# Kernel tuning notes

Hardware: AMD Instinct MI355X
Metric: run time of the kernel (lower is better)

The kernel has to match this reference:

```python
import jax, jax.numpy as jnp
import numpy as np

WS = 8          # window_size
POOL = 7        # int(sqrt(agent_num=49)) -> AdaptiveAvgPool1d output size


def _pool_matrix(L, p):
    """Averaging matrix [L, p] replicating torch AdaptiveAvgPool1d(L -> p)."""
    starts = np.floor(np.arange(p) * L / p).astype(int)
    ends = np.ceil((np.arange(p) + 1) * L / p).astype(int)
    P = np.zeros((L, p), dtype=np.float32)
    for i in range(p):
        P[starts[i]:ends[i], i] = 1.0 / (ends[i] - starts[i])
    return jnp.asarray(P)


def setup_inputs() -> dict:
    key = jax.random.key(0)
    ks = jax.random.split(key, 4)
    B, C, H, W = 8, 96, 192, 192
    s = 1.0 / np.sqrt(C)
    return {
        "x": jax.random.normal(ks[0], (B, C, H, W), jnp.float32),
        "Wv": jax.random.normal(ks[1], (C, C), jnp.float32) * s,
        "bv": jnp.zeros((C,), jnp.float32),
        "Wq": jax.random.normal(ks[2], (C, C), jnp.float32) * s,
        "bq": jnp.zeros((C,), jnp.float32),
        "Wk": jax.random.normal(ks[3], (C, C), jnp.float32) * s,
        "bk": jnp.zeros((C,), jnp.float32),
    }


def _conv1x1(x, Wt, b):
    # Conv2d(dim, dim, 1): weight [out, in]
    return jnp.einsum('bchw,oc->bohw', x, Wt) + b[None, :, None, None]


def reference(x, Wv, bv, Wq, bq, Wk, bk):
    B, C, H, W = x.shape
    ws = WS
    nh, nw = H // ws, W // ws
    L = ws * ws  # tokens per window (64)

    v = _conv1x1(x, Wv, bv)
    q = _conv1x1(x, Wq, bq)
    k = _conv1x1(x, Wk, bk)

    def win(t):  # b c (h dh) (w dw) -> (b h w) (dh dw) c
        t = t.reshape(B, C, nh, ws, nw, ws)
        return t.transpose(0, 2, 4, 3, 5, 1).reshape(B * nh * nw, L, C)

    vw, qw, kw = win(v), win(q), win(k)  # (N, 64, C) each

    # agent tokens: adaptive avg pool over the 64 in-window positions -> 7
    P = _pool_matrix(L, POOL)
    agent = jnp.einsum('nlc,lp->npc', qw, P)  # (N, 7, C)

    # agent attention (attn_drop = 0 -> identity)
    a_attn = jax.nn.softmax(jnp.einsum('npc,nlc->npl', agent, kw), axis=-1)
    agent_v = jnp.einsum('npl,nlc->npc', a_attn, vw)            # (N, 7, C)
    q_attn = jax.nn.softmax(jnp.einsum('nlc,npc->nlp', qw, agent), axis=-1)
    f = jnp.einsum('nlp,npc->nlc', q_attn, agent_v)             # (N, 64, C)

    # (b h w) (dh dw) c -> b c (h dh) (w dw)
    out = f.reshape(B, nh, nw, ws, ws, C).transpose(0, 5, 1, 3, 2, 4)
    return out.reshape(B, C, H, W)
```

## Files before the change

### kernel.cpp

```cpp
#include <hip/hip_runtime.h>


constexpr int C_   = 96;
constexpr int Wimg = 192;
constexpr int HWp  = 192 * 192;
constexpr int NWIN = 24;
constexpr int Pp   = 7;

typedef __attribute__((ext_vector_type(8))) __bf16 bf16x8;
typedef __attribute__((ext_vector_type(4))) __bf16 bf16x4;
typedef __attribute__((ext_vector_type(8))) short  short8;
typedef __attribute__((ext_vector_type(4))) float  f32x4;
union frag_u { short8 s; bf16x8 b; };

constexpr int XWS   = 0;
constexpr int RA    = 12288;
constexpr int XPH   = RA;
constexpr int XPL   = RA + 1600;
constexpr int LRAW  = RA;
constexpr int RB    = 16512;
constexpr int GKQH  = RB;
constexpr int GKQL  = RB + 3200;
constexpr int AVH   = RB;
constexpr int AVL   = RB + 1536;
constexpr int QATH  = 22912;
constexpr int QATL  = 23936;
constexpr int BIAS  = 24960;
constexpr int SMEMB = 25024;

constexpr int WS_FRAG_BYTE = 18944 * 4;
constexpr int WS_WV_BYTE   = WS_FRAG_BYTE + 84 * 1024;


__device__ __forceinline__ void bar() {
    asm volatile("s_waitcnt lgkmcnt(0)" ::: "memory");
    __builtin_amdgcn_s_barrier();
}

__device__ __forceinline__ short8 xws_fragA(const unsigned char* S, int mt, int ks, int lane) {
    const int c  = mt * 16 + (lane & 15);
    const int l2 = ks * 64 + ((lane >> 4) << 4);
    return *reinterpret_cast<const short8*>(S + XWS + c * 128 + (l2 ^ ((c & 7) << 4)));
}

__device__ __forceinline__ void pack_hilo4(unsigned char* S, int hi_off, int lo_off,
                                           const f32x4 acc) {
    bf16x4 h, l;
    #pragma unroll
    for (int i = 0; i < 4; ++i) {
        h[i] = (__bf16)acc[i];
        l[i] = (__bf16)(acc[i] - (float)h[i]);
    }
    *reinterpret_cast<bf16x4*>(S + hi_off) = h;
    *reinterpret_cast<bf16x4*>(S + lo_off) = l;
}


__global__ void precompute_mv(const float* __restrict__ Wq,
                              const float* __restrict__ Wk,
                              const float* __restrict__ bq,
                              const float* __restrict__ bk,
                              float* __restrict__ Mk,  float* __restrict__ Mq,
                              float* __restrict__ uk,  float* __restrict__ uq,
                              float* __restrict__ bk2, float* __restrict__ bq2,
                              float* __restrict__ scal)
{
    const int bid = blockIdx.x;
    if (bid < 96) {
        const int c  = bid;
        const int cp = threadIdx.x;
        float ak = 0.f, aq = 0.f;
        for (int a = 0; a < C_; ++a) {
            const float wq = Wq[a * C_ + c];
            ak = fmaf(wq, Wk[a * C_ + cp], ak);
            aq = fmaf(wq, Wq[a * C_ + cp], aq);
        }
        Mk[c * C_ + cp] = ak;
        Mq[c * C_ + cp] = aq;
    } else {
        const int c = threadIdx.x;
        float a_uk = 0.f, a_uq = 0.f, a_bk2 = 0.f, a_bq2 = 0.f;
        for (int a = 0; a < C_; ++a) {
            const float wqc = Wq[a * C_ + c];
            a_uk  = fmaf(wqc, bk[a], a_uk);
            a_uq  = fmaf(wqc, bq[a], a_uq);
            a_bk2 = fmaf(bq[a], Wk[a * C_ + c], a_bk2);
            a_bq2 = fmaf(bq[a], Wq[a * C_ + c], a_bq2);
        }
        uk[c] = a_uk; uq[c] = a_uq; bk2[c] = a_bk2; bq2[c] = a_bq2;
        if (c == 0) {
            float sk = 0.f, sq = 0.f;
            for (int a = 0; a < C_; ++a) { sk += bq[a] * bk[a]; sq += bq[a] * bq[a]; }
            scal[0] = sk; scal[1] = sq;
        }
    }
}

__global__ void precompute_frags(const float* __restrict__ ws,
                                 const float* __restrict__ Wv,
                                 unsigned char* __restrict__ wsb)
{
    const int bid = blockIdx.x, lane = threadIdx.x;
    short8 o;
    if (bid < 84) {
        const int hl = bid & 1, ks = (bid >> 1) % 3, nt = (bid / 6) % 7, mat = bid / 42;
        const float* M = ws + (mat ? 9216 : 0);
        const float* u = ws + (mat ? 18528 : 18432);
        const int col = nt * 16 + (lane & 15);
        #pragma unroll
        for (int j = 0; j < 8; ++j) {
            const int k = ks * 32 + (lane >> 4) * 8 + j;
            const float raw = (col < 96) ? M[k * 96 + col] : ((col == 96) ? u[k] : 0.f);
            const __bf16 hi = (__bf16)raw;
            union { __bf16 h; short s; } cv;
            cv.h = hl ? (__bf16)(raw - (float)hi) : hi;
            o[j] = cv.s;
        }
        *reinterpret_cast<short8*>(wsb + WS_FRAG_BYTE + bid * 1024 + lane * 16) = o;
    } else {
        const int wb = bid - 84;
        const int hl = wb & 1, ks = (wb >> 1) % 3, mt = wb / 6;
        const int row = mt * 16 + (lane & 15);
        #pragma unroll
        for (int j = 0; j < 8; ++j) {
            const int c = ks * 32 + (lane >> 4) * 8 + j;
            const float raw = Wv[row * 96 + c];
            const __bf16 hi = (__bf16)raw;
            union { __bf16 h; short s; } cv;
            cv.h = hl ? (__bf16)(raw - (float)hi) : hi;
            o[j] = cv.s;
        }
        *reinterpret_cast<short8*>(wsb + WS_WV_BYTE + wb * 1024 + lane * 16) = o;
    }
}

#define LOADPAIR(dstH, dstL, tab, slot_h) do {                                               \
    (dstH).s = *reinterpret_cast<const short8*>((tab) + (slot_h) * 1024 + (lane << 4));      \
    (dstL).s = *reinterpret_cast<const short8*>((tab) + ((slot_h) + 1) * 1024 + (lane << 4));\
} while (0)


__global__ __launch_bounds__(256, 5) void camixer_main(
    const float* __restrict__ x,
    const float* __restrict__ bv,
    const float* __restrict__ bk2,
    const float* __restrict__ bq2,
    const float* __restrict__ scal,
    const unsigned char* __restrict__ mfrag,
    const unsigned char* __restrict__ wvfrag,
    float* __restrict__ out)
{
    __shared__ __align__(16) unsigned char S[SMEMB];
    float* Lraw   = (float*)(S + LRAW);
    float* bias16 = (float*)(S + BIAS);

    const int t = threadIdx.x;
    const int lane = t & 63, w = t >> 6;
    const int wid = ((blockIdx.x & 7) * 576) + (blockIdx.x >> 3);
    const int b  = wid / (NWIN * NWIN);
    const int r  = wid % (NWIN * NWIN);
    const int h0 = (r / NWIN) * 8;
    const int w0 = (r % NWIN) * 8;
    const int base = b * C_ * HWp + h0 * Wimg + w0;
    const float scal0 = scal[0], scal1 = scal[1];
    const short8 zero8 = {0, 0, 0, 0, 0, 0, 0, 0};

    frag_u B0h[3], B0l[3];
    LOADPAIR(B0h[0], B0l[0], mfrag, (w * 3 + 0) * 2);
    LOADPAIR(B0h[1], B0l[1], mfrag, (w * 3 + 1) * 2);
    LOADPAIR(B0h[2], B0l[2], mfrag, (w * 3 + 2) * 2);

    {
        const float4* x4 = reinterpret_cast<const float4*>(x);
        #pragma unroll
        for (int rr = 0; rr < 2; ++rr) {
            const int idx = t + (rr << 8);
            if (idx < 384) {
                const int dw4 = idx & 1;
                const int dh  = (idx >> 1) & 7;
                const int c4  = idx >> 4;
                const int c0 = c4 * 4, l0 = dh * 8 + dw4 * 4;
                #pragma unroll
                for (int j = 0; j < 4; ++j) {
                    const int c = c0 + j;
                    const float4 v = x4[(base + c * HWp + dh * Wimg + dw4 * 4) >> 2];
                    bf16x4 d = {(__bf16)v.x, (__bf16)v.y, (__bf16)v.z, (__bf16)v.w};
                    *reinterpret_cast<bf16x4*>(S + XWS + c * 128 + ((l0 * 2) ^ ((c & 7) << 4))) = d;
                }
            }
        }
    }
    bar();

    {
        frag_u PBh[2], PBl[2];
        {
            const int p = lane & 15;
            const __bf16 PH = (__bf16)0.1f;
            const __bf16 PL = (__bf16)(0.1f - (float)PH);
            const int sp = (p < 7) ? ((p << 6) / 7) : 1000;
            #pragma unroll
            for (int ks = 0; ks < 2; ++ks)
                #pragma unroll
                for (int j = 0; j < 8; ++j) {
                    const int l = ks * 32 + (lane >> 4) * 8 + j;
                    const bool in = (l >= sp) && (l < sp + 10);
                    PBh[ks].b[j] = in ? PH : (__bf16)0.f;
                    PBl[ks].b[j] = in ? PL : (__bf16)0.f;
                }
        }
        #pragma unroll
        for (int rnd = 0; rnd < 2; ++rnd) {
            const int mt = rnd ? (4 + w) : w;
            if (rnd == 0 || w < 2) {
                f32x4 acc = {0.f, 0.f, 0.f, 0.f};
                #pragma unroll
                for (int ks = 0; ks < 2; ++ks) {
                    frag_u A;
                    A.s = xws_fragA(S, mt, ks, lane);
                    acc = __builtin_amdgcn_mfma_f32_16x16x32_bf16(A.b, PBh[ks].b, acc, 0, 0, 0);
                    acc = __builtin_amdgcn_mfma_f32_16x16x32_bf16(A.b, PBl[ks].b, acc, 0, 0, 0);
                }
                const int p = lane & 15;
                if (p < 8) {
                    const int c0 = mt * 16 + (lane >> 4) * 4;
                    pack_hilo4(S, XPH + p * 200 + c0 * 2, XPL + p * 200 + c0 * 2, acc);
                }
            }
        }
    }
    bar();

    {
        frag_u Bh[3], Bl[3];
        #pragma unroll
        for (int ks = 0; ks < 3; ++ks) {
            const int off = ((lane & 15) & 7) * 200 + (ks * 32 + (lane >> 4) * 8) * 2;
            Bh[ks].s = *reinterpret_cast<const short8*>(S + XPH + off);
            Bl[ks].s = *reinterpret_cast<const short8*>(S + XPL + off);
        }

        #define G0TILE(TT, AH, AL) do {                                               \
            const int tt_ = (TT);                                                     \
            const int mat_ = (tt_ >= 7) ? 1 : 0;                                      \
            const int nt_  = tt_ - 7 * mat_;                             \
            f32x4 acc = {0.f, 0.f, 0.f, 0.f};                                         \
            acc = __builtin_amdgcn_mfma_f32_16x16x32_bf16(AH[0].b, Bh[0].b, acc, 0,0,0); \
            acc = __builtin_amdgcn_mfma_f32_16x16x32_bf16(AL[0].b, Bh[0].b, acc, 0,0,0); \
            acc = __builtin_amdgcn_mfma_f32_16x16x32_bf16(AH[0].b, Bl[0].b, acc, 0,0,0); \
            acc = __builtin_amdgcn_mfma_f32_16x16x32_bf16(AH[1].b, Bh[1].b, acc, 0,0,0); \
            acc = __builtin_amdgcn_mfma_f32_16x16x32_bf16(AL[1].b, Bh[1].b, acc, 0,0,0); \
            acc = __builtin_amdgcn_mfma_f32_16x16x32_bf16(AH[1].b, Bl[1].b, acc, 0,0,0); \
            acc = __builtin_amdgcn_mfma_f32_16x16x32_bf16(AH[2].b, Bh[2].b, acc, 0,0,0); \
            acc = __builtin_amdgcn_mfma_f32_16x16x32_bf16(AL[2].b, Bh[2].b, acc, 0,0,0); \
            acc = __builtin_amdgcn_mfma_f32_16x16x32_bf16(AH[2].b, Bl[2].b, acc, 0,0,0); \
            const int p_ = lane & 15;                                    \
            if (nt_ < 6) {                                                            \
                if (p_ < 8) {                                                         \
                    const int cp0_ = nt_ * 16 + (lane >> 4) * 4;                      \
                    const float4 b4_ = *reinterpret_cast<const float4*>(              \
                        (mat_ ? bq2 : bk2) + cp0_);                                   \
                    f32x4 av_;                                                        \
                    av_[0] = acc[0] + b4_.x; av_[1] = acc[1] + b4_.y;                 \
                    av_[2] = acc[2] + b4_.z; av_[3] = acc[3] + b4_.w;                 \
                    const int pr_ = p_ + 8 * mat_;                                    \
                    pack_hilo4(S, GKQH + pr_ * 200 + cp0_ * 2,                        \
                               GKQL + pr_ * 200 + cp0_ * 2, av_);                     \
                }                                                                     \
            } else if ((lane >> 4) == 0 && p_ < 8) {                                  \
                bias16[p_ + 8 * mat_] = acc[0];             \
            }                                                                         \
        } while (0)

        frag_u B1h[3], B1l[3], B2h[3], B2l[3], B3h[3], B3l[3];
        LOADPAIR(B1h[0], B1l[0], mfrag, ((w + 4) * 3 + 0) * 2);
        LOADPAIR(B1h[1], B1l[1], mfrag, ((w + 4) * 3 + 1) * 2);
        LOADPAIR(B1h[2], B1l[2], mfrag, ((w + 4) * 3 + 2) * 2);
        G0TILE(w, B0h, B0l);
        LOADPAIR(B2h[0], B2l[0], mfrag, ((w + 8) * 3 + 0) * 2);
        LOADPAIR(B2h[1], B2l[1], mfrag, ((w + 8) * 3 + 1) * 2);
        LOADPAIR(B2h[2], B2l[2], mfrag, ((w + 8) * 3 + 2) * 2);
        G0TILE(w + 4, B1h, B1l);
        if (w < 2) {
            LOADPAIR(B3h[0], B3l[0], mfrag, ((w + 12) * 3 + 0) * 2);
            LOADPAIR(B3h[1], B3l[1], mfrag, ((w + 12) * 3 + 1) * 2);
            LOADPAIR(B3h[2], B3l[2], mfrag, ((w + 12) * 3 + 2) * 2);
        }
        G0TILE(w + 8, B2h, B2l);
        if (w < 2) G0TILE(w + 12, B3h, B3l);
        #undef G0TILE
    }
    bar();

    {
        frag_u B[3];
        {
            const int l2 = (w * 16 + (lane & 15)) * 2;
            const int kb = (lane >> 4) << 10;
            #pragma unroll
            for (int j = 0; j < 8; ++j) {
                const int aj = kb + j * 128 + (l2 ^ (j << 4));
                B[0].b[j] = *reinterpret_cast<const __bf16*>(S + XWS + aj);
                B[1].b[j] = *reinterpret_cast<const __bf16*>(S + XWS + 4096 + aj);
                B[2].b[j] = *reinterpret_cast<const __bf16*>(S + XWS + 8192 + aj);
            }
        }
        frag_u Ah[3], Al[3];
        #pragma unroll
        for (int ks = 0; ks < 3; ++ks) {
            const int off = (lane & 15) * 200 + (ks * 32 + (lane >> 4) * 8) * 2;
            Ah[ks].s = *reinterpret_cast<const short8*>(S + GKQH + off);
            Al[ks].s = *reinterpret_cast<const short8*>(S + GKQL + off);
        }
        f32x4 acc = {0.f, 0.f, 0.f, 0.f};
        #pragma unroll
        for (int ks = 0; ks < 3; ++ks) {
            acc = __builtin_amdgcn_mfma_f32_16x16x32_bf16(Ah[ks].b, B[ks].b, acc, 0, 0, 0);
            acc = __builtin_amdgcn_mfma_f32_16x16x32_bf16(Al[ks].b, B[ks].b, acc, 0, 0, 0);
        }
        const int colL = w * 16 + (lane & 15);
        const int g = lane >> 4;
        if (g < 2) {
            #pragma unroll
            for (int rr = 0; rr < 4; ++rr) {
                const int pr = g * 4 + rr;
                Lraw[pr * 66 + colL] = acc[rr] + bias16[pr] + scal0;
            }
        } else {
            const bool isg3 = (g == 3);
            float v[4];
            #pragma unroll
            for (int rr = 0; rr < 4; ++rr)
                v[rr] = acc[rr] + bias16[8 + (g - 2) * 4 + rr] + scal1;
            float mymax = fmaxf(fmaxf(v[0], v[1]), isg3 ? v[2] : fmaxf(v[2], v[3]));
            const float omax = __shfl_xor(mymax, 16);
            const float mx = fmaxf(mymax, omax);
            float e[4];
            e[0] = __expf(v[0] - mx); e[1] = __expf(v[1] - mx); e[2] = __expf(v[2] - mx);
            e[3] = isg3 ? 0.f : __expf(v[3] - mx);
            float mysum = (e[0] + e[1]) + (e[2] + e[3]);
            const float osum = __shfl_xor(mysum, 16);
            const float inv = 1.f / (mysum + osum);
            float a[4], pa[4];
            #pragma unroll
            for (int rr = 0; rr < 4; ++rr) a[rr] = e[rr] * inv;
            #pragma unroll
            for (int rr = 0; rr < 4; ++rr) pa[rr] = __shfl_xor(a[rr], 16);
            if (!isg3) {
                frag_u qh, ql;
                #pragma unroll
                for (int p = 0; p < 4; ++p) {
                    const __bf16 hb = (__bf16)a[p];
                    qh.b[p] = hb; ql.b[p] = (__bf16)(a[p] - (float)hb);
                }
                #pragma unroll
                for (int p = 0; p < 4; ++p) {
                    const __bf16 hb = (__bf16)pa[p];
                    qh.b[4 + p] = hb; ql.b[4 + p] = (__bf16)(pa[p] - (float)hb);
                }
                *reinterpret_cast<short8*>(S + QATH + colL * 16) = qh.s;
                *reinterpret_cast<short8*>(S + QATL + colL * 16) = ql.s;
            }
        }
    }
    bar();

    {
        const int nrows = (w < 3) ? 2 : 1;
        #pragma unroll
        for (int rr = 0; rr < 2; ++rr) {
            if (rr < nrows) {
                const int pp = (w < 3) ? (w + 3 * rr) : 6;
                const float v = Lraw[pp * 66 + lane];
                float mx = v;
                #pragma unroll
                for (int off = 32; off; off >>= 1) mx = fmaxf(mx, __shfl_xor(mx, off));
                const float e = __expf(v - mx);
                float s = e;
                #pragma unroll
                for (int off = 32; off; off >>= 1) s += __shfl_xor(s, off);
                const float a = e / s;
                const __bf16 hb = (__bf16)a;
                const __bf16 lb = (__bf16)(a - (float)hb);
                const int ks = lane >> 5;
                const int off_b = ((pp + 16 * ((lane >> 3) & 3)) << 4) + ((lane & 7) << 1);
                *reinterpret_cast<__bf16*>(S + RB + (ks << 10) + off_b) = hb;
                *reinterpret_cast<__bf16*>(S + RB + ((2 + ks) << 10) + off_b) = lb;
            }
        }
    }
    bar();

    frag_u V0h[3], V0l[3], V1h[3], V1l[3];
    {
        LOADPAIR(V0h[0], V0l[0], wvfrag, (w * 3 + 0) * 2);
        LOADPAIR(V0h[1], V0l[1], wvfrag, (w * 3 + 1) * 2);
        LOADPAIR(V0h[2], V0l[2], wvfrag, (w * 3 + 2) * 2);
        if (w < 2) {
            LOADPAIR(V1h[0], V1l[0], wvfrag, ((4 + w) * 3 + 0) * 2);
            LOADPAIR(V1h[1], V1l[1], wvfrag, ((4 + w) * 3 + 1) * 2);
            LOADPAIR(V1h[2], V1l[2], wvfrag, ((4 + w) * 3 + 2) * 2);
        }

        frag_u Bh[2], Bl[2];
        #pragma unroll
        for (int ks = 0; ks < 2; ++ks) {
            Bh[ks].s = *reinterpret_cast<const short8*>(S + RB + (ks << 10) + (lane << 4));
            Bl[ks].s = *reinterpret_cast<const short8*>(S + RB + ((2 + ks) << 10) + (lane << 4));
        }
        const int mt0 = (w < 2) ? w * 2 : (w + 2);
        const int nmt = (w < 2) ? 2 : 1;
        for (int m = 0; m < nmt; ++m) {
            const int mt = mt0 + m;
            f32x4 acc = {0.f, 0.f, 0.f, 0.f};
            #pragma unroll
            for (int ks = 0; ks < 2; ++ks) {
                frag_u A;
                A.s = xws_fragA(S, mt, ks, lane);
                acc = __builtin_amdgcn_mfma_f32_16x16x32_bf16(A.b, Bh[ks].b, acc, 0, 0, 0);
                acc = __builtin_amdgcn_mfma_f32_16x16x32_bf16(A.b, Bl[ks].b, acc, 0, 0, 0);
            }
            const int p = lane & 15;
            if (p < 8) {
                const int c0 = mt * 16 + (lane >> 4) * 4;
                pack_hilo4(S, XPH + p * 200 + c0 * 2, XPL + p * 200 + c0 * 2, acc);
            }
        }
    }
    bar();

    {
        const bool row7 = ((lane & 15) & 7) == 7;
        frag_u Ah[3], Al[3];
        #pragma unroll
        for (int ks = 0; ks < 3; ++ks) {
            const int off = ((lane & 15) & 7) * 200 + (ks * 32 + (lane >> 4) * 8) * 2;
            Ah[ks].s = row7 ? zero8 : *reinterpret_cast<const short8*>(S + XPH + off);
            Al[ks].s = row7 ? zero8 : *reinterpret_cast<const short8*>(S + XPL + off);
        }
        #define G3TILE(OT, VH, VL) do {                     \
            f32x4 acc = {0.f, 0.f, 0.f, 0.f};                                         \
            acc = __builtin_amdgcn_mfma_f32_16x16x32_bf16(Ah[0].b, VH[0].b, acc, 0,0,0); \
            acc = __builtin_amdgcn_mfma_f32_16x16x32_bf16(Al[0].b, VH[0].b, acc, 0,0,0); \
            acc = __builtin_amdgcn_mfma_f32_16x16x32_bf16(Ah[0].b, VL[0].b, acc, 0,0,0); \
            acc = __builtin_amdgcn_mfma_f32_16x16x32_bf16(Ah[1].b, VH[1].b, acc, 0,0,0); \
            acc = __builtin_amdgcn_mfma_f32_16x16x32_bf16(Al[1].b, VH[1].b, acc, 0,0,0); \
            acc = __builtin_amdgcn_mfma_f32_16x16x32_bf16(Ah[1].b, VL[1].b, acc, 0,0,0); \
            acc = __builtin_amdgcn_mfma_f32_16x16x32_bf16(Ah[2].b, VH[2].b, acc, 0,0,0); \
            acc = __builtin_amdgcn_mfma_f32_16x16x32_bf16(Al[2].b, VH[2].b, acc, 0,0,0); \
            acc = __builtin_amdgcn_mfma_f32_16x16x32_bf16(Ah[2].b, VL[2].b, acc, 0,0,0); \
            if ((lane >> 4) < 2) {                    \
                const int o_ = (OT) * 16 + (lane & 15);                               \
                const float bvo_ = bv[o_];                                            \
                f32x4 av_;                                                            \
                av_[0] = acc[0] + bvo_; av_[1] = acc[1] + bvo_;                       \
                av_[2] = acc[2] + bvo_; av_[3] = acc[3] + bvo_;                       \
                const int p0_ = (lane >> 4) * 4;                                      \
                pack_hilo4(S, AVH + o_ * 16 + p0_ * 2, AVL + o_ * 16 + p0_ * 2, av_); \
            }                                                                         \
        } while (0)
        G3TILE(w, V0h, V0l);
        if (w < 2) G3TILE(4 + w, V1h, V1l);
        #undef G3TILE
    }
    bar();

    {
        const int kblk = lane >> 4, nlow = lane & 15;
        const int l = w * 16 + nlow;
        frag_u Bh, Bl;
        if (kblk == 0) {
            Bh.s = *reinterpret_cast<const short8*>(S + QATH + l * 16);
            Bl.s = *reinterpret_cast<const short8*>(S + QATL + l * 16);
        } else { Bh.s = zero8; Bl.s = zero8; }
        const int obase = b * C_ * HWp + (h0 + (l >> 3)) * Wimg + w0 + (l & 7);
        #pragma unroll
        for (int mt = 0; mt < 6; ++mt) {
            frag_u Ah, Al;
            if (kblk == 0) {
                Ah.s = *reinterpret_cast<const short8*>(S + AVH + (mt * 16 + nlow) * 16);
                Al.s = *reinterpret_cast<const short8*>(S + AVL + (mt * 16 + nlow) * 16);
            } else { Ah.s = zero8; Al.s = zero8; }
            f32x4 acc = {0.f, 0.f, 0.f, 0.f};
            acc = __builtin_amdgcn_mfma_f32_16x16x32_bf16(Ah.b, Bh.b, acc, 0, 0, 0);
            acc = __builtin_amdgcn_mfma_f32_16x16x32_bf16(Ah.b, Bl.b, acc, 0, 0, 0);
            acc = __builtin_amdgcn_mfma_f32_16x16x32_bf16(Al.b, Bh.b, acc, 0, 0, 0);
            #pragma unroll
            for (int rr = 0; rr < 4; ++rr) {
                const int o = mt * 16 + kblk * 4 + rr;
                out[obase + o * HWp] = acc[rr];
            }
        }
    }
}


extern "C" void kernel_launch(void* const* d_in, const int* in_sizes, int n_in,
                              void* d_out, int out_size, void* d_ws, size_t ws_size,
                              hipStream_t stream)
{
    const float* x  = (const float*)d_in[0];
    const float* Wv = (const float*)d_in[1];
    const float* bv = (const float*)d_in[2];
    const float* Wq = (const float*)d_in[3];
    const float* bq = (const float*)d_in[4];
    const float* Wk = (const float*)d_in[5];
    const float* bk = (const float*)d_in[6];
    float* out = (float*)d_out;

    float* ws = (float*)d_ws;
    float* Mk   = ws;
    float* Mq   = ws + 9216;
    float* uk   = ws + 18432;
    float* uq   = ws + 18528;
    float* bk2  = ws + 18624;
    float* bq2  = ws + 18720;
    float* scal = ws + 18816;
    unsigned char* wsb = (unsigned char*)d_ws;

    hipLaunchKernelGGL(precompute_mv, dim3(97), dim3(C_), 0, stream,
                       Wq, Wk, bq, bk, Mk, Mq, uk, uq, bk2, bq2, scal);
    hipLaunchKernelGGL(precompute_frags, dim3(120), dim3(64), 0, stream,
                       ws, Wv, wsb);
    hipLaunchKernelGGL(camixer_main, dim3(8 * NWIN * NWIN), dim3(256), 0, stream,
                       x, bv, bk2, bq2, scal,
                       wsb + WS_FRAG_BYTE, wsb + WS_WV_BYTE, out);
}
```

Before: 72.12 us.

## Keep agent_v fragments in registers and drop LDS round-trip and barrier

The agent_v tile from the third GEMM is no longer stored to LDS and reread by other waves. Each wave now rebuilds its hi/lo bf16 A-fragments in registers through a cross-lane shuffle and then computes the final output for its own channel tiles across all 64 tokens. This removes one LDS write/read pass and a block barrier. In exchange, output work is split by channel tile instead of by token, so waves 0-1 do twice the MFMA and store work of waves 2-3, and the store pattern per wave changes.

Result: no change. 71.79 us (median of 2 runs) (-0.5%).

```diff
diff --git a/kernel.cpp b/kernel.cpp
--- a/kernel.cpp
+++ b/kernel.cpp
@@ -21,8 +21,6 @@
 constexpr int RB    = 16512;
 constexpr int GKQH  = RB;
 constexpr int GKQL  = RB + 3200;
-constexpr int AVH   = RB;
-constexpr int AVL   = RB + 1536;
 constexpr int QATH  = 22912;
 constexpr int QATL  = 23936;
 constexpr int BIAS  = 24960;
@@ -438,7 +436,9 @@
             Ah[ks].s = row7 ? zero8 : *reinterpret_cast<const short8*>(S + XPH + off);
             Al[ks].s = row7 ? zero8 : *reinterpret_cast<const short8*>(S + XPL + off);
         }
-        #define G3TILE(OT, VH, VL) do {                     \
+
+        frag_u PA0h, PA0l, PA1h, PA1l;
+        #define G3ACC(OT, VH, VL, DSTH, DSTL) do {                                    \
             f32x4 acc = {0.f, 0.f, 0.f, 0.f};                                         \
             acc = __builtin_amdgcn_mfma_f32_16x16x32_bf16(Ah[0].b, VH[0].b, acc, 0,0,0); \
             acc = __builtin_amdgcn_mfma_f32_16x16x32_bf16(Al[0].b, VH[0].b, acc, 0,0,0); \
@@ -449,46 +449,56 @@
             acc = __builtin_amdgcn_mfma_f32_16x16x32_bf16(Ah[2].b, VH[2].b, acc, 0,0,0); \
             acc = __builtin_amdgcn_mfma_f32_16x16x32_bf16(Al[2].b, VH[2].b, acc, 0,0,0); \
             acc = __builtin_amdgcn_mfma_f32_16x16x32_bf16(Ah[2].b, VL[2].b, acc, 0,0,0); \
-            if ((lane >> 4) < 2) {                    \
-                const int o_ = (OT) * 16 + (lane & 15);                               \
-                const float bvo_ = bv[o_];                                            \
-                f32x4 av_;                                                            \
-                av_[0] = acc[0] + bvo_; av_[1] = acc[1] + bvo_;                       \
-                av_[2] = acc[2] + bvo_; av_[3] = acc[3] + bvo_;                       \
-                const int p0_ = (lane >> 4) * 4;                                      \
-                pack_hilo4(S, AVH + o_ * 16 + p0_ * 2, AVL + o_ * 16 + p0_ * 2, av_); \
-            }                                                                         \
+            float p47[4];                                                             \
+            _Pragma("unroll")                                                         \
+            for (int rr = 0; rr < 4; ++rr) p47[rr] = __shfl_xor(acc[rr], 16);         \
+            if ((lane >> 4) == 0) {                                                   \
+                const float bvo_ = bv[(OT) * 16 + (lane & 15)];                       \
+                float vv[8] = {acc[0] + bvo_, acc[1] + bvo_, acc[2] + bvo_,           \
+                               acc[3] + bvo_, p47[0] + bvo_, p47[1] + bvo_,           \
+                               p47[2] + bvo_, p47[3] + bvo_};                         \
+                _Pragma("unroll")                                                     \
+                for (int j = 0; j < 8; ++j) {                                         \
+                    const __bf16 hb = (__bf16)vv[j];                                  \
+                    (DSTH).b[j] = hb;                                                 \
+                    (DSTL).b[j] = (__bf16)(vv[j] - (float)hb);                        \
+                }                                                                     \
+            } else { (DSTH).s = zero8; (DSTL).s = zero8; }                            \
         } while (0)
-        G3TILE(w, V0h, V0l);
-        if (w < 2) G3TILE(4 + w, V1h, V1l);
-        #undef G3TILE
-    }
-    bar();
-
-    {
-        const int kblk = lane >> 4, nlow = lane & 15;
-        const int l = w * 16 + nlow;
-        frag_u Bh, Bl;
-        if (kblk == 0) {
-            Bh.s = *reinterpret_cast<const short8*>(S + QATH + l * 16);
-            Bl.s = *reinterpret_cast<const short8*>(S + QATL + l * 16);
-        } else { Bh.s = zero8; Bl.s = zero8; }
-        const int obase = b * C_ * HWp + (h0 + (l >> 3)) * Wimg + w0 + (l & 7);
-        #pragma unroll
-        for (int mt = 0; mt < 6; ++mt) {
-            frag_u Ah, Al;
-            if (kblk == 0) {
-                Ah.s = *reinterpret_cast<const short8*>(S + AVH + (mt * 16 + nlow) * 16);
-                Al.s = *reinterpret_cast<const short8*>(S + AVL + (mt * 16 + nlow) * 16);
-            } else { Ah.s = zero8; Al.s = zero8; }
-            f32x4 acc = {0.f, 0.f, 0.f, 0.f};
-            acc = __builtin_amdgcn_mfma_f32_16x16x32_bf16(Ah.b, Bh.b, acc, 0, 0, 0);
-            acc = __builtin_amdgcn_mfma_f32_16x16x32_bf16(Ah.b, Bl.b, acc, 0, 0, 0);
-            acc = __builtin_amdgcn_mfma_f32_16x16x32_bf16(Al.b, Bh.b, acc, 0, 0, 0);
-            #pragma unroll
-            for (int rr = 0; rr < 4; ++rr) {
-                const int o = mt * 16 + kblk * 4 + rr;
-                out[obase + o * HWp] = acc[rr];
+        G3ACC(w, V0h, V0l, PA0h, PA0l);
+        if (w < 2) G3ACC(4 + w, V1h, V1l, PA1h, PA1l);
+        #undef G3ACC
+
+        #pragma unroll
+        for (int lt = 0; lt < 4; ++lt) {
+            const int ll = lt * 16 + (lane & 15);
+            frag_u Bh, Bl;
+            if ((lane >> 4) == 0) {
+                Bh.s = *reinterpret_cast<const short8*>(S + QATH + ll * 16);
+                Bl.s = *reinterpret_cast<const short8*>(S + QATL + ll * 16);
+            } else { Bh.s = zero8; Bl.s = zero8; }
+            const int obase = b * C_ * HWp + (h0 + (ll >> 3)) * Wimg + w0 + (ll & 7);
+            {
+                f32x4 a0 = {0.f, 0.f, 0.f, 0.f};
+                a0 = __builtin_amdgcn_mfma_f32_16x16x32_bf16(PA0h.b, Bh.b, a0, 0, 0, 0);
+                a0 = __builtin_amdgcn_mfma_f32_16x16x32_bf16(PA0h.b, Bl.b, a0, 0, 0, 0);
+                a0 = __builtin_amdgcn_mfma_f32_16x16x32_bf16(PA0l.b, Bh.b, a0, 0, 0, 0);
+                #pragma unroll
+                for (int rr = 0; rr < 4; ++rr) {
+                    const int o = w * 16 + (lane >> 4) * 4 + rr;
+                    out[obase + o * HWp] = a0[rr];
+                }
+            }
+            if (w < 2) {
+                f32x4 a1 = {0.f, 0.f, 0.f, 0.f};
+                a1 = __builtin_amdgcn_mfma_f32_16x16x32_bf16(PA1h.b, Bh.b, a1, 0, 0, 0);
+                a1 = __builtin_amdgcn_mfma_f32_16x16x32_bf16(PA1h.b, Bl.b, a1, 0, 0, 0);
+                a1 = __builtin_amdgcn_mfma_f32_16x16x32_bf16(PA1l.b, Bh.b, a1, 0, 0, 0);
+                #pragma unroll
+                for (int rr = 0; rr < 4; ++rr) {
+                    const int o = (4 + w) * 16 + (lane >> 4) * 4 + rr;
+                    out[obase + o * HWp] = a1[rr];
+                }
             }
         }
     }
```
